# Kernel optimization log

Measured on AMD Instinct MI355X. Metric: run time of the kernel, lower is better.

## Reference

```python
import jax, jax.numpy as jnp
import numpy as np

D = 1024      # d_model
H = 16        # nhead
DH = D // H   # head_dim = 64
ROT = DH // 2 # rotary_ndims = 32
FFN = 4096    # d_ffn
B, T, M, N = 4, 1024, 128, 64


def _layernorm(x, g, b, eps=1e-5):
    mu = jnp.mean(x, axis=-1, keepdims=True)
    var = jnp.mean(jnp.square(x - mu), axis=-1, keepdims=True)
    return (x - mu) * jax.lax.rsqrt(var + eps) * g + b


def _rotate_half(x):
    x1, x2 = x[..., : x.shape[-1] // 2], x[..., x.shape[-1] // 2:]
    return jnp.concatenate([-x2, x1], axis=-1)


def setup_inputs() -> dict:
    key = jax.random.key(0)
    ks = jax.random.split(key, 16)
    s = 0.02
    inp = {
        'x': jax.random.normal(ks[0], (B, T, D), jnp.float32),
        'memory': jax.random.normal(ks[1], (B, M, D), jnp.float32),
        'nmr': jax.random.normal(ks[2], (B, N, D), jnp.float32),
        'Wq': jax.random.normal(ks[3], (D, D), jnp.float32) * s,
        'bq': jnp.zeros((D,), jnp.float32),
        'Wk': jax.random.normal(ks[4], (D, D), jnp.float32) * s,
        'bk': jnp.zeros((D,), jnp.float32),
        'Wv': jax.random.normal(ks[5], (D, D), jnp.float32) * s,
        'bv': jnp.zeros((D,), jnp.float32),
        'Wo': jax.random.normal(ks[6], (D, D), jnp.float32) * s,
        'bo': jnp.zeros((D,), jnp.float32),
        'W1': jax.random.normal(ks[7], (D, FFN), jnp.float32) * s,
        'b1': jnp.zeros((FFN,), jnp.float32),
        'W2': jax.random.normal(ks[8], (FFN, D), jnp.float32) * s,
        'b2': jnp.zeros((D,), jnp.float32),
        'ln1_g': jnp.ones((D,), jnp.float32),
        'ln1_b': jnp.zeros((D,), jnp.float32),
        'ln2_g': jnp.ones((D,), jnp.float32),
        'ln2_b': jnp.zeros((D,), jnp.float32),
    }
    return inp


def reference(x, memory, nmr, Wq, bq, Wk, bk, Wv, bv, Wo, bo, W1, b1, W2, b2,
              ln1_g, ln1_b, ln2_g, ln2_b):
    b, t, _ = x.shape
    m, n = memory.shape[1], nmr.shape[1]
    pref = m + n
    L = pref + t

    x_full = jnp.concatenate([memory, nmr, x], axis=1)  # (B, L, D)
    xa = _layernorm(x_full, ln1_g, ln1_b)

    def heads(w, bias):
        return (xa @ w + bias).reshape(b, L, H, DH).transpose(0, 2, 1, 3)  # (B,H,L,DH)

    q = heads(Wq, bq)
    k = heads(Wk, bk)
    v = heads(Wv, bv)

    # partial RoPE on first ROT dims of each head
    pos = jnp.arange(L, dtype=jnp.float32)
    inv_freq = 1.0 / (10000.0 ** (jnp.arange(0, ROT, 2, dtype=jnp.float32) / ROT))
    freqs = pos[:, None] * inv_freq[None, :]              # (L, ROT/2)
    emb = jnp.concatenate([freqs, freqs], axis=-1)        # (L, ROT)
    cos, sin = jnp.cos(emb), jnp.sin(emb)
    qr, qp = q[..., :ROT], q[..., ROT:]
    kr, kp = k[..., :ROT], k[..., ROT:]
    qr = qr * cos + _rotate_half(qr) * sin
    kr = kr * cos + _rotate_half(kr) * sin
    q = jnp.concatenate([qr, qp], axis=-1)
    k = jnp.concatenate([kr, kp], axis=-1)

    # block mask: prefix (memory+nmr) fully bidirectional, target causal,
    # target attends to full prefix, prefix does NOT attend to target.
    i = jnp.arange(L)
    allowed = (i[None, :] < pref) | ((i[:, None] >= pref) & (i[None, :] >= pref)
                                     & (i[None, :] <= i[:, None]))  # (L, L)

    scale = 1.0 / jnp.sqrt(jnp.asarray(DH, jnp.float32))
    scores = jnp.einsum('bhqd,bhkd->bhqk', q, k) * scale
    scores = jnp.where(allowed[None, None], scores, jnp.finfo(scores.dtype).min)
    probs = jax.nn.softmax(scores, axis=-1)
    attn = jnp.einsum('bhqk,bhkd->bhqd', probs, v)        # (B,H,L,DH)
    attn = attn.transpose(0, 2, 1, 3).reshape(b, L, D)

    x_full = attn @ Wo + bo + x_full

    xf = _layernorm(x_full, ln2_g, ln2_b)
    xf = jnp.square(jax.nn.relu(xf @ W1 + b1)) @ W2 + b2
    x_full = x_full + xf

    return x_full[:, pref:]
```

## Files before the change

kernel.cpp:

```cpp
#include <hip/hip_runtime.h>
#include <hip/hip_bf16.h>
#include <math.h>

#define D_   1024
#define H_   16
#define DH_  64
#define FFN_ 4096
#define B_   4
#define T_   1024
#define M_   128
#define N_   64
#define PREF 192
#define L_   1216
#define BL_  (B_*L_)
#define BT_  (B_*T_)

typedef __attribute__((ext_vector_type(4))) float f32x4;
typedef __attribute__((ext_vector_type(8))) short bf16x8;
typedef __attribute__((ext_vector_type(8))) unsigned short u16x8;
typedef const __attribute__((address_space(1))) void gvoid_t;
typedef __attribute__((address_space(3))) void lvoid_t;

#define LGKM0 asm volatile("s_waitcnt lgkmcnt(0)" ::: "memory")

__device__ __forceinline__ void gl_lds16(const void* g, void* l) {
    __builtin_amdgcn_global_load_lds((gvoid_t*)g, (lvoid_t*)l, 16, 0, 0);
}

__device__ __forceinline__ ushort f2bf(float x) {
    union { __hip_bfloat16 h; ushort u; } cv;
    cv.h = __float2bfloat16(x);
    return cv.u;
}

__device__ __forceinline__ u16x8 pack8(float4 a, float4 b) {
    u16x8 r;
    r[0]=f2bf(a.x); r[1]=f2bf(a.y); r[2]=f2bf(a.z); r[3]=f2bf(a.w);
    r[4]=f2bf(b.x); r[5]=f2bf(b.y); r[6]=f2bf(b.z); r[7]=f2bf(b.w);
    return r;
}

__device__ __forceinline__ float block_reduce_sum256(float v, float* sbuf) {
#pragma unroll
    for (int o = 32; o > 0; o >>= 1) v += __shfl_xor(v, o, 64);
    int w = threadIdx.x >> 6;
    if ((threadIdx.x & 63) == 0) sbuf[w] = v;
    __syncthreads();
    float r = sbuf[0] + sbuf[1] + sbuf[2] + sbuf[3];
    __syncthreads();
    return r;
}

__device__ __forceinline__ void wtr_body(const float* __restrict__ W,
                                         ushort* __restrict__ Wt, int K, int Nc)
{
    __shared__ float tl[64][65];
    int c0 = blockIdx.x << 6, k0 = blockIdx.y << 6;
    int tid = threadIdx.x;
    int rr = tid >> 4, c4 = (tid & 15) << 2;
#pragma unroll
    for (int p = 0; p < 4; ++p) {
        int r = (p << 4) + rr;
        float4 v = *(const float4*)(W + (size_t)(k0 + r) * Nc + c0 + c4);
        tl[r][c4+0] = v.x; tl[r][c4+1] = v.y; tl[r][c4+2] = v.z; tl[r][c4+3] = v.w;
    }
    __syncthreads();
#pragma unroll
    for (int p = 0; p < 4; ++p) {
        int rT = (p << 4) + rr;
        ushort4 uv;
        uv.x = f2bf(tl[c4+0][rT]);
        uv.y = f2bf(tl[c4+1][rT]);
        uv.z = f2bf(tl[c4+2][rT]);
        uv.w = f2bf(tl[c4+3][rT]);
        *(ushort4*)(Wt + (size_t)(c0 + rT) * K + k0 + c4) = uv;
    }
}

__global__ __launch_bounds__(256) void wtr_kernel(
    const float* __restrict__ W, ushort* __restrict__ Wt, int K, int Nc)
{ wtr_body(W, Wt, K, Nc); }

__global__ __launch_bounds__(256) void wtr4_kernel(
    const float* __restrict__ W0, const float* __restrict__ W1,
    const float* __restrict__ W2, const float* __restrict__ W3,
    ushort* __restrict__ T0, ushort* __restrict__ T1,
    ushort* __restrict__ T2, ushort* __restrict__ T3)
{
    const float* W; ushort* T;
    switch (blockIdx.z) {
        case 0: W = W0; T = T0; break;
        case 1: W = W1; T = T1; break;
        case 2: W = W2; T = T2; break;
        default: W = W3; T = T3; break;
    }
    wtr_body(W, T, D_, D_);
}

__global__ __launch_bounds__(256) void prep_kernel(
    float* __restrict__ tab, const float* __restrict__ bq,
    const float* __restrict__ bk, const float* __restrict__ bv,
    float* __restrict__ ob)
{
    int i = blockIdx.x * 256 + threadIdx.x;
    if (i < L_ * 32) {
        int pos = i >> 5, idx = i & 31;
        int fi = idx & 15;
        float invf = exp2f(-(float)fi * 0.83048202372f);
        float th = (float)pos * invf;
        tab[i] = (idx < 16) ? cosf(th) : sinf(th);
    } else {
        int j = i - L_ * 32;
        if (j < 3072) {
            float v = (j < 1024) ? bq[j] : (j < 2048 ? bk[j - 1024] : bv[j - 2048]);
            ob[j] = v;
        }
    }
}

__global__ __launch_bounds__(256) void ln1_concat_kernel(
    const float* __restrict__ x, const float* __restrict__ mem,
    const float* __restrict__ nmr, const float* __restrict__ g,
    const float* __restrict__ be, float* __restrict__ x_full,
    ushort* __restrict__ xa_bf)
{
    __shared__ float sbuf[4];
    int row = blockIdx.x;
    int b = row / L_, pos = row % L_;
    const float* src;
    if (pos < M_)          src = mem + ((size_t)b*M_ + pos)      * D_;
    else if (pos < M_+N_)  src = nmr + ((size_t)b*N_ + (pos-M_)) * D_;
    else                   src = x   + ((size_t)b*T_ + (pos-PREF))*D_;

    int c = threadIdx.x << 2;
    float4 v = *(const float4*)(src + c);
    float s = v.x + v.y + v.z + v.w;
    s = block_reduce_sum256(s, sbuf);
    float mu = s * (1.0f / D_);
    float dx = v.x - mu, dy = v.y - mu, dz = v.z - mu, dw = v.w - mu;
    float q = dx*dx + dy*dy + dz*dz + dw*dw;
    q = block_reduce_sum256(q, sbuf);
    float inv = rsqrtf(q * (1.0f / D_) + 1e-5f);
    float4 gv = *(const float4*)(g + c);
    float4 bv = *(const float4*)(be + c);
    ushort4 o;
    o.x = f2bf(dx*inv*gv.x + bv.x);
    o.y = f2bf(dy*inv*gv.y + bv.y);
    o.z = f2bf(dz*inv*gv.z + bv.z);
    o.w = f2bf(dw*inv*gv.w + bv.w);
    *(float4*)(x_full + (size_t)row*D_ + c) = v;
    *(ushort4*)(xa_bf + (size_t)row*D_ + c) = o;
}

__global__ __launch_bounds__(256) void ln2_kernel(
    const float* __restrict__ src, const float* __restrict__ g,
    const float* __restrict__ be, ushort* __restrict__ dst)
{
    __shared__ float sbuf[4];
    int row = blockIdx.x;
    int c = threadIdx.x << 2;
    float4 v = *(const float4*)(src + (size_t)row*D_ + c);
    float s = v.x + v.y + v.z + v.w;
    s = block_reduce_sum256(s, sbuf);
    float mu = s * (1.0f / D_);
    float dx = v.x - mu, dy = v.y - mu, dz = v.z - mu, dw = v.w - mu;
    float q = dx*dx + dy*dy + dz*dz + dw*dw;
    q = block_reduce_sum256(q, sbuf);
    float inv = rsqrtf(q * (1.0f / D_) + 1e-5f);
    float4 gv = *(const float4*)(g + c);
    float4 bv = *(const float4*)(be + c);
    ushort4 o;
    o.x = f2bf(dx*inv*gv.x + bv.x);
    o.y = f2bf(dy*inv*gv.y + bv.y);
    o.z = f2bf(dz*inv*gv.z + bv.z);
    o.w = f2bf(dw*inv*gv.w + bv.w);
    *(ushort4*)(dst + (size_t)row*D_ + c) = o;
}

__global__ __launch_bounds__(256) void gemm_bf16_kernel(
    const ushort* __restrict__ A, const ushort* __restrict__ Bt,
    const float* __restrict__ bias, const float* __restrict__ rtab,
    void* __restrict__ Cout, int Nc, int Kstride, int Klen, int mode)
{
    __shared__ ushort SM[16384];
    int tid = threadIdx.x;
    int lane = tid & 63, w = tid >> 6;
    int wm = w >> 1, wn = w & 1;
    int nx = gridDim.x;
    int flat = blockIdx.y * nx + blockIdx.x;
    int cpx = (nx * gridDim.y) >> 3;
    int sz = (flat & 7) * cpx + (flat >> 3);
    int row0 = (sz / nx) << 7, col0 = (sz % nx) << 7;
    int l15 = lane & 15, l4 = lane >> 4;

    f32x4 acc[4][4] = {};

    int r_a = tid >> 2;
    int sc  = tid & 3;
    int lcOff = (sc ^ ((r_a >> 1) & 3)) << 3;
    const ushort* Arow  = A  + (size_t)(row0 + r_a)      * Kstride;
    const ushort* Arow2 = A  + (size_t)(row0 + 64 + r_a) * Kstride;
    const ushort* Brow  = Bt + (size_t)(col0 + r_a)      * Kstride;
    const ushort* Brow2 = Bt + (size_t)(col0 + 64 + r_a) * Kstride;

#define STAGE(buf, k0rel)                                                          \
    do {                                                                           \
        gl_lds16(Arow  + (k0rel) + lcOff, (char*)(SM + (buf)*4096) + (tid << 4));  \
        gl_lds16(Arow2 + (k0rel) + lcOff, (char*)(SM + (buf)*4096) + ((256+tid) << 4)); \
        gl_lds16(Brow  + (k0rel) + lcOff, (char*)(SM + 8192 + (buf)*4096) + (tid << 4)); \
        gl_lds16(Brow2 + (k0rel) + lcOff, (char*)(SM + 8192 + (buf)*4096) + ((256+tid) << 4)); \
    } while (0)

    STAGE(0, 0);
    __syncthreads();
    int cur = 0;
    for (int k0 = 0; k0 < Klen; k0 += 32) {
        if (k0 + 32 < Klen) STAGE(cur ^ 1, k0 + 32);
        const ushort* As = SM + cur*4096;
        const ushort* Bs = SM + 8192 + cur*4096;
        bf16x8 af[4], bfr[4];
#pragma unroll
        for (int i = 0; i < 4; ++i) {
            int ra = (wm << 6) + (i << 4) + l15;
            af[i]  = *(const bf16x8*)(&As[ra*32 + ((l4 ^ ((ra >> 1) & 3)) << 3)]);
            int rb = (wn << 6) + (i << 4) + l15;
            bfr[i] = *(const bf16x8*)(&Bs[rb*32 + ((l4 ^ ((rb >> 1) & 3)) << 3)]);
        }
#pragma unroll
        for (int i = 0; i < 4; ++i)
#pragma unroll
            for (int j = 0; j < 4; ++j)
                acc[i][j] = __builtin_amdgcn_mfma_f32_16x16x32_bf16(af[i], bfr[j], acc[i][j], 0, 0, 0);
        __syncthreads();
        cur ^= 1;
    }
#undef STAGE

    float bcol[4];
#pragma unroll
    for (int j = 0; j < 4; ++j) bcol[j] = bias[col0 + (wn << 6) + (j << 4) + l15];

    float* scr = (float*)SM + w * 1088;
    int rr = lane >> 2, cseg = lane & 3;
    int hh = ((col0 & 1023) + (wn << 6)) >> 6;
    int which = col0 >> 10;

#pragma unroll
    for (int i = 0; i < 4; ++i) {
        LGKM0;
#pragma unroll
        for (int j = 0; j < 4; ++j)
#pragma unroll
            for (int r = 0; r < 4; ++r)
                scr[((l4 << 2) + r)*68 + (j << 4) + l15] = acc[i][j][r] + bcol[j];
        LGKM0;
        int grow = row0 + (wm << 6) + (i << 4) + rr;

        if (which == 2) {
            int r0g = row0 + (wm << 6) + (i << 4);
            int bb = r0g / L_;
            int posb = r0g - bb * L_;
            float4 v0, v1, v2, v3;
            v0.x = scr[ 0*68 + lane]; v0.y = scr[ 1*68 + lane];
            v0.z = scr[ 2*68 + lane]; v0.w = scr[ 3*68 + lane];
            v1.x = scr[ 4*68 + lane]; v1.y = scr[ 5*68 + lane];
            v1.z = scr[ 6*68 + lane]; v1.w = scr[ 7*68 + lane];
            v2.x = scr[ 8*68 + lane]; v2.y = scr[ 9*68 + lane];
            v2.z = scr[10*68 + lane]; v2.w = scr[11*68 + lane];
            v3.x = scr[12*68 + lane]; v3.y = scr[13*68 + lane];
            v3.z = scr[14*68 + lane]; v3.w = scr[15*68 + lane];
            ushort* O = (ushort*)Cout + 2*(size_t)BL_*D_;
            size_t base = ((size_t)(bb*H_ + hh)*64 + lane)*L_ + posb;
            *(u16x8*)(O + base)     = pack8(v0, v1);
            *(u16x8*)(O + base + 8) = pack8(v2, v3);
        } else {
            int bb = grow / L_;
            int pos = grow - bb * L_;
            float4 a0 = *(float4*)&scr[rr*68 + (cseg << 4) + 0];
            float4 a1 = *(float4*)&scr[rr*68 + (cseg << 4) + 4];
            float4 a2 = *(float4*)&scr[rr*68 + (cseg << 4) + 8];
            float4 a3 = *(float4*)&scr[rr*68 + (cseg << 4) + 12];
            if (cseg < 2) {
                int oseg = cseg ^ 1;
                float4 p0 = *(float4*)&scr[rr*68 + (oseg << 4) + 0];
                float4 p1 = *(float4*)&scr[rr*68 + (oseg << 4) + 4];
                float4 p2 = *(float4*)&scr[rr*68 + (oseg << 4) + 8];
                float4 p3 = *(float4*)&scr[rr*68 + (oseg << 4) + 12];
                const float* tb = rtab + pos*32;
                float4 c0 = *(const float4*)(tb + 0),  c1 = *(const float4*)(tb + 4);
                float4 c2 = *(const float4*)(tb + 8),  c3 = *(const float4*)(tb + 12);
                float4 s0 = *(const float4*)(tb + 16), s1 = *(const float4*)(tb + 20);
                float4 s2 = *(const float4*)(tb + 24), s3 = *(const float4*)(tb + 28);
                float sg = (cseg == 0) ? -1.f : 1.f;
                a0.x = a0.x*c0.x + sg*p0.x*s0.x; a0.y = a0.y*c0.y + sg*p0.y*s0.y;
                a0.z = a0.z*c0.z + sg*p0.z*s0.z; a0.w = a0.w*c0.w + sg*p0.w*s0.w;
                a1.x = a1.x*c1.x + sg*p1.x*s1.x; a1.y = a1.y*c1.y + sg*p1.y*s1.y;
                a1.z = a1.z*c1.z + sg*p1.z*s1.z; a1.w = a1.w*c1.w + sg*p1.w*s1.w;
                a2.x = a2.x*c2.x + sg*p2.x*s2.x; a2.y = a2.y*c2.y + sg*p2.y*s2.y;
                a2.z = a2.z*c2.z + sg*p2.z*s2.z; a2.w = a2.w*c2.w + sg*p2.w*s2.w;
                a3.x = a3.x*c3.x + sg*p3.x*s3.x; a3.y = a3.y*c3.y + sg*p3.y*s3.y;
                a3.z = a3.z*c3.z + sg*p3.z*s3.z; a3.w = a3.w*c3.w + sg*p3.w*s3.w;
            }
            ushort* O = (ushort*)Cout + (size_t)which * ((size_t)BL_*D_);
            size_t base = (((size_t)(bb*H_ + hh)*L_ + pos) << 6) + (cseg << 4);
            *(u16x8*)(O + base)     = pack8(a0, a1);
            *(u16x8*)(O + base + 8) = pack8(a2, a3);
        }
    }
}

__global__ __launch_bounds__(512) void gemm_ffn1_kernel(
    const ushort* __restrict__ A, const ushort* __restrict__ Bt,
    const float* __restrict__ bias, void* __restrict__ Cout,
    int Nc, int Kstride, int Klen)
{
    __shared__ ushort SM[24576];
    char* SMb = (char*)SM;

    int tid = threadIdx.x;
    int lane = tid & 63, w = tid >> 6;
    int l15 = lane & 15, l4 = lane >> 4;

    int nx = gridDim.x;
    int flat = blockIdx.y * nx + blockIdx.x;
    int cpx = (nx * gridDim.y) >> 3;
    int sz = (flat & 7) * cpx + (flat >> 3);
    int row0 = (sz / nx) << 7, col0 = (sz % nx) << 8;

    int wm = w >> 2, wn = w & 3;

    f32x4 acc[4][4] = {};

    int rA = tid >> 2, scA = tid & 3;
    int lcA = (scA ^ ((rA >> 1) & 3)) << 3;
    const ushort* Ar = A + (size_t)(row0 + rA) * Kstride + lcA;
    int lcB1 = (scA ^ (((128 + rA) >> 1) & 3)) << 3;
    const ushort* Br0 = Bt + (size_t)(col0 + rA)       * Kstride + lcA;
    const ushort* Br1 = Bt + (size_t)(col0 + 128 + rA) * Kstride + lcB1;
#define STG1(buf, k0rel)                                                        \
    do {                                                                        \
        gl_lds16(Ar  + (k0rel), SMb + (buf)*8192 + (tid << 4));                 \
        gl_lds16(Br0 + (k0rel), SMb + 16384 + (buf)*16384 + (tid << 4));        \
        gl_lds16(Br1 + (k0rel), SMb + 16384 + (buf)*16384 + 8192 + (tid << 4)); \
    } while (0)
    STG1(0, 0);
    __syncthreads();
    int cur = 0;
    for (int k0 = 0; k0 < Klen; k0 += 32) {
        if (k0 + 32 < Klen) STG1(cur ^ 1, k0 + 32);
        const ushort* As = (const ushort*)(SMb + cur*8192);
        const ushort* Bs = (const ushort*)(SMb + 16384 + cur*16384);
        bf16x8 af[4], bfr[4];
#pragma unroll
        for (int i = 0; i < 4; ++i) {
            int ra = (wm << 6) + (i << 4) + l15;
            af[i]  = *(const bf16x8*)(&As[ra*32 + ((l4 ^ ((ra >> 1) & 3)) << 3)]);
            int rb = (wn << 6) + (i << 4) + l15;
            bfr[i] = *(const bf16x8*)(&Bs[rb*32 + ((l4 ^ ((rb >> 1) & 3)) << 3)]);
        }
#pragma unroll
        for (int i = 0; i < 4; ++i)
#pragma unroll
            for (int j = 0; j < 4; ++j)
                acc[i][j] = __builtin_amdgcn_mfma_f32_16x16x32_bf16(af[i], bfr[j], acc[i][j], 0, 0, 0);
        __syncthreads();
        cur ^= 1;
    }
#undef STG1

    float bcol[4];
#pragma unroll
    for (int j = 0; j < 4; ++j) bcol[j] = bias[col0 + (wn << 6) + (j << 4) + l15];

    float* scr = (float*)SMb + w * 1088;
    int rr = lane >> 2, cseg = lane & 3;
    int colbase = col0 + (wn << 6);

#pragma unroll
    for (int i = 0; i < 4; ++i) {
        LGKM0;
#pragma unroll
        for (int j = 0; j < 4; ++j)
#pragma unroll
            for (int r = 0; r < 4; ++r) {
                float v = acc[i][j][r] + bcol[j];
                v = fmaxf(v, 0.f); v *= v;
                scr[((l4 << 2) + r)*68 + (j << 4) + l15] = v;
            }
        LGKM0;
        int grow = row0 + (wm << 6) + (i << 4) + rr;
        float4 q0 = *(float4*)&scr[rr*68 + (cseg << 4) + 0];
        float4 q1 = *(float4*)&scr[rr*68 + (cseg << 4) + 4];
        float4 q2 = *(float4*)&scr[rr*68 + (cseg << 4) + 8];
        float4 q3 = *(float4*)&scr[rr*68 + (cseg << 4) + 12];
        int gcol = colbase + (cseg << 4);
        ushort* O = (ushort*)Cout;
        *(u16x8*)(O + (size_t)grow*Nc + gcol)     = pack8(q0, q1);
        *(u16x8*)(O + (size_t)grow*Nc + gcol + 8) = pack8(q2, q3);
    }
}

__global__ __launch_bounds__(256) void gemm_sk2_kernel(
    const ushort* __restrict__ A, const ushort* __restrict__ Bt,
    const float* __restrict__ bias, const float* __restrict__ res,
    float* __restrict__ Cout, int Nc, int Kstride, int Klen, int mode)
{
    __shared__ ushort SM[24576];
    char* SMb = (char*)SM;
    int tid = threadIdx.x;
    int lane = tid & 63, w = tid >> 6;
    int l15 = lane & 15, l4 = lane >> 4;
    int g = w >> 1, wm = w & 1;

    int nx = gridDim.x;
    int flat = blockIdx.y * nx + blockIdx.x;
    int cpx = (nx * gridDim.y) >> 3;
    int sz = (flat & 7) * cpx + (flat >> 3);
    int row0 = (sz / nx) << 7, col0 = (sz % nx) << 6;

    f32x4 acc[4][4] = {};
    const int kl = Klen >> 1;
    const int kb = g * kl;

    int gt = tid & 127;
    int rB = gt >> 2, sc = gt & 3;
    const ushort* Abase = A  + (size_t)row0 * Kstride + kb;
    const ushort* Bbase = Bt + (size_t)col0 * Kstride + kb;
    char* AL = SMb + g * 16384;
    char* BL = SMb + 32768 + g * 8192;

#define STG2(buf, k0rel)                                                        \
    do {                                                                        \
        _Pragma("unroll")                                                       \
        for (int p = 0; p < 4; ++p) {                                           \
            int rw = (p << 5) + rB; int lc = sc ^ ((rw >> 1) & 3);              \
            gl_lds16(Abase + (size_t)rw*Kstride + (k0rel) + (lc << 3),          \
                     AL + (buf)*8192 + (p << 11) + (gt << 4));                  \
        }                                                                       \
        _Pragma("unroll")                                                       \
        for (int p = 0; p < 2; ++p) {                                           \
            int rw = (p << 5) + rB; int lc = sc ^ ((rw >> 1) & 3);              \
            gl_lds16(Bbase + (size_t)rw*Kstride + (k0rel) + (lc << 3),          \
                     BL + (buf)*4096 + (p << 11) + (gt << 4));                  \
        }                                                                       \
    } while (0)

    STG2(0, 0);
    __syncthreads();
    int cur = 0;
    for (int k0 = 0; k0 < kl; k0 += 32) {
        if (k0 + 32 < kl) STG2(cur ^ 1, k0 + 32);
        const ushort* As = (const ushort*)(AL + cur*8192);
        const ushort* Bs = (const ushort*)(BL + cur*4096);
        bf16x8 af[4], bfr[4];
#pragma unroll
        for (int i = 0; i < 4; ++i) {
            int ra = (wm << 6) + (i << 4) + l15;
            af[i]  = *(const bf16x8*)(&As[ra*32 + ((l4 ^ ((ra >> 1) & 3)) << 3)]);
            int rb = (i << 4) + l15;
            bfr[i] = *(const bf16x8*)(&Bs[rb*32 + ((l4 ^ ((rb >> 1) & 3)) << 3)]);
        }
#pragma unroll
        for (int i = 0; i < 4; ++i)
#pragma unroll
            for (int j = 0; j < 4; ++j)
                acc[i][j] = __builtin_amdgcn_mfma_f32_16x16x32_bf16(af[i], bfr[j], acc[i][j], 0, 0, 0);
        __syncthreads();
        cur ^= 1;
    }
#undef STG2

    float* scr2 = (float*)SMb;
    if (g == 1) {
#pragma unroll
        for (int i = 0; i < 4; ++i)
#pragma unroll
            for (int j = 0; j < 4; ++j)
#pragma unroll
                for (int r = 0; r < 4; ++r)
                    scr2[((wm << 6) + (i << 4) + (l4 << 2) + r)*68 + (j << 4) + l15] = acc[i][j][r];
    }
    __syncthreads();
    if (g == 1) return;
#pragma unroll
    for (int i = 0; i < 4; ++i)
#pragma unroll
        for (int j = 0; j < 4; ++j)
#pragma unroll
            for (int r = 0; r < 4; ++r)
                acc[i][j][r] += scr2[((wm << 6) + (i << 4) + (l4 << 2) + r)*68 + (j << 4) + l15];

    float bcol[4];
#pragma unroll
    for (int j = 0; j < 4; ++j) bcol[j] = bias[col0 + (j << 4) + l15];
    int rr = lane >> 2, cseg = lane & 3;
    float* scr = (float*)(SMb + 36864) + w * 1088;

#pragma unroll
    for (int i = 0; i < 4; ++i) {
        LGKM0;
#pragma unroll
        for (int j = 0; j < 4; ++j)
#pragma unroll
            for (int r = 0; r < 4; ++r)
                scr[((l4 << 2) + r)*68 + (j << 4) + l15] = acc[i][j][r] + bcol[j];
        LGKM0;
        int grow = row0 + (wm << 6) + (i << 4) + rr;
        float4 q0 = *(float4*)&scr[rr*68 + (cseg << 4) + 0];
        float4 q1 = *(float4*)&scr[rr*68 + (cseg << 4) + 4];
        float4 q2 = *(float4*)&scr[rr*68 + (cseg << 4) + 8];
        float4 q3 = *(float4*)&scr[rr*68 + (cseg << 4) + 12];
        int gcol = col0 + (cseg << 4);
        size_t roff;
        if (mode == 2) {
            int rs = (grow >> 10)*L_ + PREF + (grow & (T_-1));
            roff = (size_t)rs*D_ + gcol;
        } else {
            roff = (size_t)grow*Nc + gcol;
        }
        float4 r0 = *(const float4*)(res + roff);
        float4 r1 = *(const float4*)(res + roff + 4);
        float4 r2 = *(const float4*)(res + roff + 8);
        float4 r3 = *(const float4*)(res + roff + 12);
        q0.x += r0.x; q0.y += r0.y; q0.z += r0.z; q0.w += r0.w;
        q1.x += r1.x; q1.y += r1.y; q1.z += r1.z; q1.w += r1.w;
        q2.x += r2.x; q2.y += r2.y; q2.z += r2.z; q2.w += r2.w;
        q3.x += r3.x; q3.y += r3.y; q3.z += r3.z; q3.w += r3.w;
        size_t o = (size_t)grow*Nc + gcol;
        *(float4*)(Cout + o)      = q0;
        *(float4*)(Cout + o + 4)  = q1;
        *(float4*)(Cout + o + 8)  = q2;
        *(float4*)(Cout + o + 12) = q3;
    }
}

__global__ __launch_bounds__(256) void attn_mfma_kernel(
    const ushort* __restrict__ qhd, const ushort* __restrict__ khd,
    const ushort* __restrict__ vt, ushort* __restrict__ attn_bf)
{
    __shared__ ushort Ks[2][64*64];
    __shared__ ushort Vs[2][64*64];
    __shared__ ushort Ps[4*16*64];

    int bid0 = blockIdx.x;
    int bid = (bid0 & 7) * (gridDim.x >> 3) + (bid0 >> 3);
    int qb = 15 - (bid & 15);
    int h  = (bid >> 4) & (H_ - 1);
    int b  = bid >> 8;
    int tid = threadIdx.x, lane = tid & 63, w = tid >> 6;
    int l15 = lane & 15, lg = lane >> 4;
    int i0 = PREF + (qb << 6);
    int wq0 = w << 4;
    size_t bh = (size_t)(b * H_ + h);

    const ushort* qrow = qhd + (bh * L_ + i0 + wq0 + l15) * 64;
    bf16x8 bq0 = *(const bf16x8*)(qrow + (lg << 3));
    bf16x8 bq1 = *(const bf16x8*)(qrow + 32 + (lg << 3));

    f32x4 acc[4] = {};
    float mrun = -INFINITY;
    float lsum = 0.f;

    int srow = tid >> 3;
    int sslot = tid & 7;
    ushort* Ps_w = Ps + (w << 10);
    const float SC = 0.125f * 1.4426950408889634f;
    int qcap = i0 + wq0 + l15;

#define STAGE_T(buf, t)                                                     \
    do { int j0s = (t) << 6;                                                \
        gl_lds16(khd + (bh * L_ + j0s + srow) * 64 + ((sslot ^ (srow & 7)) << 3),      \
                 (char*)Ks[buf] + (tid << 4));                              \
        gl_lds16(khd + (bh * L_ + j0s + 32 + srow) * 64 + ((sslot ^ ((32+srow) & 7)) << 3), \
                 (char*)Ks[buf] + ((256 + tid) << 4));                      \
        gl_lds16(vt + (bh * 64 + srow) * L_ + j0s + ((sslot ^ (srow & 7)) << 3),       \
                 (char*)Vs[buf] + (tid << 4));                              \
        gl_lds16(vt + (bh * 64 + 32 + srow) * L_ + j0s + ((sslot ^ ((32+srow) & 7)) << 3), \
                 (char*)Vs[buf] + ((256 + tid) << 4));                      \
    } while (0)

    int ntile = 4 + qb;
    STAGE_T(0, 0);
    __syncthreads();
    int cur = 0;
    for (int t = 0; t < ntile; ++t) {
        if (t + 1 < ntile) STAGE_T(cur ^ 1, t + 1);
        const ushort* Kc = Ks[cur];
        const ushort* Vc = Vs[cur];

        f32x4 s4[4];
        __builtin_amdgcn_s_setprio(1);
#pragma unroll
        for (int st = 0; st < 4; ++st) {
            int rk = (st << 4) + l15;
            bf16x8 ak0 = *(const bf16x8*)(Kc + (rk << 6) + ((lg       ^ (rk & 7)) << 3));
            bf16x8 ak1 = *(const bf16x8*)(Kc + (rk << 6) + (((4 + lg) ^ (rk & 7)) << 3));
            f32x4 z = {};
            z = __builtin_amdgcn_mfma_f32_16x16x32_bf16(ak0, bq0, z, 0, 0, 0);
            z = __builtin_amdgcn_mfma_f32_16x16x32_bf16(ak1, bq1, z, 0, 0, 0);
            s4[st] = z;
        }
        __builtin_amdgcn_s_setprio(0);

        int j0 = t << 6;
        float sv[4][4];
        bool diag = (t == ntile - 1);
        int kbq = j0 + (lg << 2);
#pragma unroll
        for (int st = 0; st < 4; ++st)
#pragma unroll
            for (int r = 0; r < 4; ++r) {
                float s = s4[st][r] * SC;
                if (diag && (kbq + (st << 4) + r > qcap)) s = -INFINITY;
                sv[st][r] = s;
            }
        float bm;
        {
            float t0 = fmaxf(fmaxf(sv[0][0], sv[0][1]), fmaxf(sv[0][2], sv[0][3]));
            float t1 = fmaxf(fmaxf(sv[1][0], sv[1][1]), fmaxf(sv[1][2], sv[1][3]));
            float t2 = fmaxf(fmaxf(sv[2][0], sv[2][1]), fmaxf(sv[2][2], sv[2][3]));
            float t3 = fmaxf(fmaxf(sv[3][0], sv[3][1]), fmaxf(sv[3][2], sv[3][3]));
            bm = fmaxf(fmaxf(t0, t1), fmaxf(t2, t3));
        }
        bm = fmaxf(bm, __shfl_xor(bm, 16, 64));
        bm = fmaxf(bm, __shfl_xor(bm, 32, 64));

        float mn = fmaxf(mrun, bm);
        float cr = exp2f(mrun - mn);
        mrun = mn;
        float pe[4][4];
        float ps = 0.f;
#pragma unroll
        for (int st = 0; st < 4; ++st)
#pragma unroll
            for (int r = 0; r < 4; ++r) {
                float e = exp2f(sv[st][r] - mn);
                pe[st][r] = e; ps += e;
            }
        ps += __shfl_xor(ps, 16, 64);
        ps += __shfl_xor(ps, 32, 64);
        lsum = lsum * cr + ps;
#pragma unroll
        for (int su = 0; su < 4; ++su) acc[su] *= cr;

#pragma unroll
        for (int st = 0; st < 4; ++st) {
            int slot = (st << 1) + (lg >> 1);
            int sb = ((lg & 1) << 3);
#pragma unroll
            for (int rp = 0; rp < 2; ++rp) {
                uint u = (uint)f2bf(pe[st][2*rp]) | ((uint)f2bf(pe[st][2*rp+1]) << 16);
                *(uint*)((char*)Ps_w + l15*128 + ((slot ^ (l15 & 7)) << 4) + sb + (rp << 2)) = u;
            }
        }
        {
            bf16x8 bp0 = *(const bf16x8*)((char*)Ps_w + l15*128 + ((lg       ^ (l15 & 7)) << 4));
            bf16x8 bp1 = *(const bf16x8*)((char*)Ps_w + l15*128 + (((4 + lg) ^ (l15 & 7)) << 4));
            __builtin_amdgcn_s_setprio(1);
#pragma unroll
            for (int su = 0; su < 4; ++su) {
                int rd = (su << 4) + l15;
                bf16x8 av0 = *(const bf16x8*)(Vc + (rd << 6) + ((lg       ^ (rd & 7)) << 3));
                bf16x8 av1 = *(const bf16x8*)(Vc + (rd << 6) + (((4 + lg) ^ (rd & 7)) << 3));
                acc[su] = __builtin_amdgcn_mfma_f32_16x16x32_bf16(av0, bp0, acc[su], 0, 0, 0);
                acc[su] = __builtin_amdgcn_mfma_f32_16x16x32_bf16(av1, bp1, acc[su], 0, 0, 0);
            }
            __builtin_amdgcn_s_setprio(0);
        }
        __syncthreads();
        cur ^= 1;
    }
#undef STAGE_T

    float rl = 1.0f / lsum;
    size_t orow = (size_t)b * T_ + (i0 - PREF) + wq0 + l15;
#pragma unroll
    for (int su = 0; su < 4; ++su) {
        ushort4 o4;
        o4.x = f2bf(acc[su][0] * rl);
        o4.y = f2bf(acc[su][1] * rl);
        o4.z = f2bf(acc[su][2] * rl);
        o4.w = f2bf(acc[su][3] * rl);
        *(ushort4*)(attn_bf + orow * D_ + (h << 6) + (su << 4) + (lg << 2)) = o4;
    }
}

extern "C" void kernel_launch(void* const* d_in, const int* in_sizes, int n_in,
                              void* d_out, int out_size, void* d_ws, size_t ws_size,
                              hipStream_t stream) {
    const float* x   = (const float*)d_in[0];
    const float* mem = (const float*)d_in[1];
    const float* nmr = (const float*)d_in[2];
    const float* Wq  = (const float*)d_in[3];
    const float* bq  = (const float*)d_in[4];
    const float* Wk  = (const float*)d_in[5];
    const float* bk  = (const float*)d_in[6];
    const float* Wv  = (const float*)d_in[7];
    const float* bv  = (const float*)d_in[8];
    const float* Wo  = (const float*)d_in[9];
    const float* bo  = (const float*)d_in[10];
    const float* W1  = (const float*)d_in[11];
    const float* b1  = (const float*)d_in[12];
    const float* W2  = (const float*)d_in[13];
    const float* b2  = (const float*)d_in[14];
    const float* g1  = (const float*)d_in[15];
    const float* be1 = (const float*)d_in[16];
    const float* g2  = (const float*)d_in[17];
    const float* be2 = (const float*)d_in[18];
    float* out = (float*)d_out;

    const size_t BLD = (size_t)BL_ * D_;
    const size_t BTD = (size_t)BT_ * D_;

    float* f = (float*)d_ws;
    float* x_full = f;
    float* x2     = f + BLD;
    float* bqkv   = x2 + BTD;
    float* rtab   = bqkv + 4096;
    ushort* bfb   = (ushort*)(rtab + (size_t)L_*32);
    ushort* xa_bf   = bfb;
    ushort* qhd     = bfb + BLD;
    ushort* khd     = bfb + 2*BLD;
    ushort* vt      = bfb + 3*BLD;
    ushort* h1_bf   = bfb + 4*BLD;
    ushort* wq_bf = h1_bf + (size_t)BT_*FFN_;
    ushort* wk_bf = wq_bf + (size_t)D_*D_;
    ushort* wv_bf = wk_bf + (size_t)D_*D_;
    ushort* wo_bf = wv_bf + (size_t)D_*D_;
    ushort* w1_bf = wo_bf + (size_t)D_*D_;
    ushort* w2_bf = w1_bf + (size_t)D_*FFN_;
    ushort* attn_bf = xa_bf;
    ushort* ln2_bf  = qhd;

    wtr4_kernel<<<dim3(16, 16, 4), 256, 0, stream>>>(Wq, Wk, Wv, Wo,
                                                     wq_bf, wk_bf, wv_bf, wo_bf);
    wtr_kernel<<<dim3(FFN_/64, D_/64),   256, 0, stream>>>(W1, w1_bf, D_,   FFN_);
    wtr_kernel<<<dim3(D_/64,   FFN_/64), 256, 0, stream>>>(W2, w2_bf, FFN_, D_);
    prep_kernel<<<(L_*32 + 3072 + 255)/256, 256, 0, stream>>>(rtab, bq, bk, bv, bqkv);

    ln1_concat_kernel<<<BL_, 256, 0, stream>>>(x, mem, nmr, g1, be1, x_full, xa_bf);

    gemm_bf16_kernel<<<dim3(3072/128, BL_/128), 256, 0, stream>>>(
        xa_bf, wq_bf, bqkv, rtab, qhd, D_, D_, D_, 7);

    attn_mfma_kernel<<<B_*H_*(T_/64), 256, 0, stream>>>(qhd, khd, vt, attn_bf);

    gemm_sk2_kernel<<<dim3(D_/64, BT_/128), 256, 0, stream>>>(
        attn_bf, wo_bf, bo, x_full, x2, D_, D_, D_, 2);

    ln2_kernel<<<BT_, 256, 0, stream>>>(x2, g2, be2, ln2_bf);

    gemm_ffn1_kernel<<<dim3(FFN_/256, BT_/128), 512, 0, stream>>>(
        ln2_bf, w1_bf, b1, h1_bf, FFN_, D_, D_);

    gemm_sk2_kernel<<<dim3(D_/64, BT_/128), 256, 0, stream>>>(
        h1_bf, w2_bf, b2, x2, out, D_, FFN_, FFN_, 1);
}
```

Measured before the change: 254.5 us.

## Triple-buffer LDS staging in GEMM kernels with explicit vmcnt waits

Converts the double-buffered global-to-LDS staging in the three GEMM kernels into a three-stage ring buffer. Loads now run two K-steps ahead, with explicit s_waitcnt vmcnt counts and raw s_barrier calls replacing __syncthreads. The goal is to hide more global load latency behind MFMA work. In exchange, LDS use grows, which may lower occupancy, and correctness now depends on the hand-tuned vmcnt counts.

```diff
diff --git a/kernel.cpp b/kernel.cpp
--- a/kernel.cpp
+++ b/kernel.cpp
@@ -22,6 +22,7 @@
 typedef __attribute__((address_space(3))) void lvoid_t;
 
 #define LGKM0 asm volatile("s_waitcnt lgkmcnt(0)" ::: "memory")
+#define CFENCE asm volatile("" ::: "memory")
 
 __device__ __forceinline__ void gl_lds16(const void* g, void* l) {
     __builtin_amdgcn_global_load_lds((gvoid_t*)g, (lvoid_t*)l, 16, 0, 0);
@@ -182,7 +183,8 @@
     const float* __restrict__ bias, const float* __restrict__ rtab,
     void* __restrict__ Cout, int Nc, int Kstride, int Klen, int mode)
 {
-    __shared__ ushort SM[16384];
+    __shared__ ushort SM[24576];
+    char* SMb = (char*)SM;
     int tid = threadIdx.x;
     int lane = tid & 63, w = tid >> 6;
     int wm = w >> 1, wn = w & 1;
@@ -203,21 +205,32 @@
     const ushort* Brow  = Bt + (size_t)(col0 + r_a)      * Kstride;
     const ushort* Brow2 = Bt + (size_t)(col0 + 64 + r_a) * Kstride;
 
-#define STAGE(buf, k0rel)                                                          \
-    do {                                                                           \
-        gl_lds16(Arow  + (k0rel) + lcOff, (char*)(SM + (buf)*4096) + (tid << 4));  \
-        gl_lds16(Arow2 + (k0rel) + lcOff, (char*)(SM + (buf)*4096) + ((256+tid) << 4)); \
-        gl_lds16(Brow  + (k0rel) + lcOff, (char*)(SM + 8192 + (buf)*4096) + (tid << 4)); \
-        gl_lds16(Brow2 + (k0rel) + lcOff, (char*)(SM + 8192 + (buf)*4096) + ((256+tid) << 4)); \
+#define STAGEQ(bb, k0rel)                                                    \
+    do { char* Ab = SMb + (bb)*8192; char* Bb = SMb + 24576 + (bb)*8192;     \
+        gl_lds16(Arow  + (k0rel) + lcOff, Ab + (tid << 4));                  \
+        gl_lds16(Arow2 + (k0rel) + lcOff, Ab + 4096 + (tid << 4));           \
+        gl_lds16(Brow  + (k0rel) + lcOff, Bb + (tid << 4));                  \
+        gl_lds16(Brow2 + (k0rel) + lcOff, Bb + 4096 + (tid << 4));           \
     } while (0)
 
-    STAGE(0, 0);
-    __syncthreads();
+    int nIt = Klen >> 5;
+    STAGEQ(0, 0);
+    STAGEQ(1, 32);
     int cur = 0;
-    for (int k0 = 0; k0 < Klen; k0 += 32) {
-        if (k0 + 32 < Klen) STAGE(cur ^ 1, k0 + 32);
-        const ushort* As = SM + cur*4096;
-        const ushort* Bs = SM + 8192 + cur*4096;
+    for (int it = 0; it < nIt; ++it) {
+        if (it + 2 < nIt) {
+            int s2 = cur + 2; if (s2 >= 3) s2 -= 3;
+            STAGEQ(s2, (it + 2) << 5);
+            asm volatile("s_waitcnt vmcnt(8)" ::: "memory");
+        } else if (it + 1 < nIt) {
+            asm volatile("s_waitcnt vmcnt(4)" ::: "memory");
+        } else {
+            asm volatile("s_waitcnt vmcnt(0)" ::: "memory");
+        }
+        __builtin_amdgcn_s_barrier();
+        CFENCE;
+        const ushort* As = (const ushort*)(SMb + cur*8192);
+        const ushort* Bs = (const ushort*)(SMb + 24576 + cur*8192);
         bf16x8 af[4], bfr[4];
 #pragma unroll
         for (int i = 0; i < 4; ++i) {
@@ -231,10 +244,11 @@
 #pragma unroll
             for (int j = 0; j < 4; ++j)
                 acc[i][j] = __builtin_amdgcn_mfma_f32_16x16x32_bf16(af[i], bfr[j], acc[i][j], 0, 0, 0);
-        __syncthreads();
-        cur ^= 1;
-    }
-#undef STAGE
+        CFENCE;
+        __builtin_amdgcn_s_barrier();
+        cur = (cur + 1 == 3) ? 0 : cur + 1;
+    }
+#undef STAGEQ
 
     float bcol[4];
 #pragma unroll
@@ -314,7 +328,7 @@
     const float* __restrict__ bias, void* __restrict__ Cout,
     int Nc, int Kstride, int Klen)
 {
-    __shared__ ushort SM[24576];
+    __shared__ ushort SM[36864];
     char* SMb = (char*)SM;
 
     int tid = threadIdx.x;
@@ -337,19 +351,32 @@
     int lcB1 = (scA ^ (((128 + rA) >> 1) & 3)) << 3;
     const ushort* Br0 = Bt + (size_t)(col0 + rA)       * Kstride + lcA;
     const ushort* Br1 = Bt + (size_t)(col0 + 128 + rA) * Kstride + lcB1;
-#define STG1(buf, k0rel)                                                        \
-    do {                                                                        \
-        gl_lds16(Ar  + (k0rel), SMb + (buf)*8192 + (tid << 4));                 \
-        gl_lds16(Br0 + (k0rel), SMb + 16384 + (buf)*16384 + (tid << 4));        \
-        gl_lds16(Br1 + (k0rel), SMb + 16384 + (buf)*16384 + 8192 + (tid << 4)); \
+
+#define STG1(bb, k0rel)                                                       \
+    do {                                                                      \
+        gl_lds16(Ar  + (k0rel), SMb + (bb)*8192 + (tid << 4));                \
+        gl_lds16(Br0 + (k0rel), SMb + 24576 + (bb)*16384 + (tid << 4));       \
+        gl_lds16(Br1 + (k0rel), SMb + 24576 + (bb)*16384 + 8192 + (tid << 4));\
     } while (0)
+
+    int nIt = Klen >> 5;
     STG1(0, 0);
-    __syncthreads();
+    STG1(1, 32);
     int cur = 0;
-    for (int k0 = 0; k0 < Klen; k0 += 32) {
-        if (k0 + 32 < Klen) STG1(cur ^ 1, k0 + 32);
+    for (int it = 0; it < nIt; ++it) {
+        if (it + 2 < nIt) {
+            int s2 = cur + 2; if (s2 >= 3) s2 -= 3;
+            STG1(s2, (it + 2) << 5);
+            asm volatile("s_waitcnt vmcnt(6)" ::: "memory");
+        } else if (it + 1 < nIt) {
+            asm volatile("s_waitcnt vmcnt(3)" ::: "memory");
+        } else {
+            asm volatile("s_waitcnt vmcnt(0)" ::: "memory");
+        }
+        __builtin_amdgcn_s_barrier();
+        CFENCE;
         const ushort* As = (const ushort*)(SMb + cur*8192);
-        const ushort* Bs = (const ushort*)(SMb + 16384 + cur*16384);
+        const ushort* Bs = (const ushort*)(SMb + 24576 + cur*16384);
         bf16x8 af[4], bfr[4];
 #pragma unroll
         for (int i = 0; i < 4; ++i) {
@@ -363,8 +390,9 @@
 #pragma unroll
             for (int j = 0; j < 4; ++j)
                 acc[i][j] = __builtin_amdgcn_mfma_f32_16x16x32_bf16(af[i], bfr[j], acc[i][j], 0, 0, 0);
-        __syncthreads();
-        cur ^= 1;
+        CFENCE;
+        __builtin_amdgcn_s_barrier();
+        cur = (cur + 1 == 3) ? 0 : cur + 1;
     }
 #undef STG1
 
@@ -405,7 +433,7 @@
     const float* __restrict__ bias, const float* __restrict__ res,
     float* __restrict__ Cout, int Nc, int Kstride, int Klen, int mode)
 {
-    __shared__ ushort SM[24576];
+    __shared__ ushort SM[36864];
     char* SMb = (char*)SM;
     int tid = threadIdx.x;
     int lane = tid & 63, w = tid >> 6;
@@ -426,32 +454,43 @@
     int rB = gt >> 2, sc = gt & 3;
     const ushort* Abase = A  + (size_t)row0 * Kstride + kb;
     const ushort* Bbase = Bt + (size_t)col0 * Kstride + kb;
-    char* AL = SMb + g * 16384;
-    char* BL = SMb + 32768 + g * 8192;
-
-#define STG2(buf, k0rel)                                                        \
-    do {                                                                        \
-        _Pragma("unroll")                                                       \
-        for (int p = 0; p < 4; ++p) {                                           \
-            int rw = (p << 5) + rB; int lc = sc ^ ((rw >> 1) & 3);              \
-            gl_lds16(Abase + (size_t)rw*Kstride + (k0rel) + (lc << 3),          \
-                     AL + (buf)*8192 + (p << 11) + (gt << 4));                  \
-        }                                                                       \
-        _Pragma("unroll")                                                       \
-        for (int p = 0; p < 2; ++p) {                                           \
-            int rw = (p << 5) + rB; int lc = sc ^ ((rw >> 1) & 3);              \
-            gl_lds16(Bbase + (size_t)rw*Kstride + (k0rel) + (lc << 3),          \
-                     BL + (buf)*4096 + (p << 11) + (gt << 4));                  \
-        }                                                                       \
+    char* ALg = SMb + g * 24576;
+    char* BLg = SMb + 49152 + g * 12288;
+
+#define STG2(bb, k0rel)                                                       \
+    do {                                                                      \
+        _Pragma("unroll")                                                     \
+        for (int p = 0; p < 4; ++p) {                                         \
+            int rw = (p << 5) + rB; int lc = sc ^ ((rw >> 1) & 3);            \
+            gl_lds16(Abase + (size_t)rw*Kstride + (k0rel) + (lc << 3),        \
+                     ALg + (bb)*8192 + (p << 11) + (gt << 4));                \
+        }                                                                     \
+        _Pragma("unroll")                                                     \
+        for (int p = 0; p < 2; ++p) {                                         \
+            int rw = (p << 5) + rB; int lc = sc ^ ((rw >> 1) & 3);            \
+            gl_lds16(Bbase + (size_t)rw*Kstride + (k0rel) + (lc << 3),        \
+                     BLg + (bb)*4096 + (p << 11) + (gt << 4));                \
+        }                                                                     \
     } while (0)
 
+    int nIt = kl >> 5;
     STG2(0, 0);
-    __syncthreads();
+    STG2(1, 32);
     int cur = 0;
-    for (int k0 = 0; k0 < kl; k0 += 32) {
-        if (k0 + 32 < kl) STG2(cur ^ 1, k0 + 32);
-        const ushort* As = (const ushort*)(AL + cur*8192);
-        const ushort* Bs = (const ushort*)(BL + cur*4096);
+    for (int it = 0; it < nIt; ++it) {
+        if (it + 2 < nIt) {
+            int s2 = cur + 2; if (s2 >= 3) s2 -= 3;
+            STG2(s2, (it + 2) << 5);
+            asm volatile("s_waitcnt vmcnt(12)" ::: "memory");
+        } else if (it + 1 < nIt) {
+            asm volatile("s_waitcnt vmcnt(6)" ::: "memory");
+        } else {
+            asm volatile("s_waitcnt vmcnt(0)" ::: "memory");
+        }
+        __builtin_amdgcn_s_barrier();
+        CFENCE;
+        const ushort* As = (const ushort*)(ALg + cur*8192);
+        const ushort* Bs = (const ushort*)(BLg + cur*4096);
         bf16x8 af[4], bfr[4];
 #pragma unroll
         for (int i = 0; i < 4; ++i) {
@@ -465,8 +504,9 @@
 #pragma unroll
             for (int j = 0; j < 4; ++j)
                 acc[i][j] = __builtin_amdgcn_mfma_f32_16x16x32_bf16(af[i], bfr[j], acc[i][j], 0, 0, 0);
-        __syncthreads();
-        cur ^= 1;
+        CFENCE;
+        __builtin_amdgcn_s_barrier();
+        cur = (cur + 1 == 3) ? 0 : cur + 1;
     }
 #undef STG2
 
```

Measured after the change: 250.4 us. About the same (-1.6%).
